# Performance work log

Hardware: AMD Instinct MI355X
Metric: run time of the kernel (lower is better)

The kernel has to match this reference:

```python
import jax, jax.numpy as jnp
import numpy as np

NEG_SLOPE = 0.2  # PyG GATConv default


def gat_conv(x, edge_index, W, a_src, a_dst, bias):
    """Single-head PyG-style GATConv (eval mode, add_self_loops=True)."""
    N = x.shape[0]
    h = x @ W  # [N, F_out]
    # add self loops
    loops = jnp.arange(N, dtype=edge_index.dtype)
    src = jnp.concatenate([edge_index[0], loops])  # [E+N]
    dst = jnp.concatenate([edge_index[1], loops])
    # per-edge attention logits: a_src . h_j + a_dst . h_i  (j=src, i=dst)
    alpha_s = h @ a_src  # [N]
    alpha_d = h @ a_dst  # [N]
    e = jax.nn.leaky_relu(alpha_s[src] + alpha_d[dst], NEG_SLOPE)  # [E+N]
    # segment softmax over incoming edges of each dst node
    m = jax.ops.segment_max(e, dst, num_segments=N)
    ex = jnp.exp(e - m[dst])
    denom = jax.ops.segment_sum(ex, dst, num_segments=N)
    alpha = ex / denom[dst]  # [E+N]
    # weighted scatter-aggregate of source features
    out = jax.ops.segment_sum(h[src] * alpha[:, None], dst, num_segments=N)
    return out + bias


def setup_inputs() -> dict:
    key = jax.random.key(0)
    ks = jax.random.split(key, 12)
    N, E = 100000, 3200000
    Fin, H, Fout = 128, 32, 32
    x = jax.random.normal(ks[0], (N, Fin), dtype=jnp.float32)
    edge_index = jax.random.randint(ks[1], (2, E), 0, N, dtype=jnp.int64)
    s = 1.0 / np.sqrt(Fin)
    W1 = jax.random.uniform(ks[2], (Fin, H), jnp.float32, -s, s)
    a1s = jax.random.uniform(ks[3], (H,), jnp.float32, -s, s)
    a1d = jax.random.uniform(ks[4], (H,), jnp.float32, -s, s)
    b1 = jnp.zeros((H,), jnp.float32)
    s2 = 1.0 / np.sqrt(H)
    W2 = jax.random.uniform(ks[5], (H, H), jnp.float32, -s2, s2)
    a2s = jax.random.uniform(ks[6], (H,), jnp.float32, -s2, s2)
    a2d = jax.random.uniform(ks[7], (H,), jnp.float32, -s2, s2)
    b2 = jnp.zeros((H,), jnp.float32)
    Wf = jax.random.uniform(ks[8], (H, Fout), jnp.float32, -s2, s2)
    bf = jax.random.uniform(ks[9], (Fout,), jnp.float32, -s2, s2)
    return {"x": x, "edge_index": edge_index, "W1": W1, "a1s": a1s, "a1d": a1d,
            "b1": b1, "W2": W2, "a2s": a2s, "a2d": a2d, "b2": b2,
            "Wf": Wf, "bf": bf}


def reference(x, edge_index, W1, a1s, a1d, b1, W2, a2s, a2d, b2, Wf, bf):
    h = jax.nn.relu(gat_conv(x, edge_index, W1, a1s, a1d, b1))
    h = jax.nn.relu(gat_conv(h, edge_index, W2, a2s, a2d, b2))
    return h @ Wf + bf
```

## Files before the change

kernel.cpp:

```cpp
#include <hip/hip_runtime.h>

#define NEG_SLOPE 0.2f
#define BK_LOG 9
#define BK_NODES (1 << BK_LOG)
#define TILE_EPT 24
#define TILE_E (256 * TILE_EPT)

typedef __attribute__((ext_vector_type(8))) short bf8_t;
typedef __attribute__((ext_vector_type(4))) float f32x4;

__device__ __forceinline__ float leaky(float v) { return v > 0.0f ? v : NEG_SLOPE * v; }

__device__ __forceinline__ unsigned short f2bf(float f) {
    unsigned u = __float_as_uint(f);
    u += 0x7fffu + ((u >> 16) & 1u);
    return (unsigned short)(u >> 16);
}
__device__ __forceinline__ float bf2f(unsigned short h) {
    return __uint_as_float(((unsigned)h) << 16);
}

__device__ __forceinline__ int scan256_excl(int v, int* tmp) {
    int t = threadIdx.x;
    tmp[t] = v;
    __syncthreads();
    for (int d = 1; d < 256; d <<= 1) {
        int x = (t >= d) ? tmp[t - d] : 0;
        __syncthreads();
        tmp[t] += x;
        __syncthreads();
    }
    int r = tmp[t] - v;
    __syncthreads();
    return r;
}

__device__ __forceinline__ void wsplit_body(int blk, int tid,
                                            const float* __restrict__ W,
                                            unsigned short* __restrict__ wh,
                                            unsigned short* __restrict__ wl, int K) {
    int idx = blk * 256 + tid;
    int KT = K >> 5;
    if (idx >= KT * 128) return;
    int lane = idx & 63;
    int nt = (idx >> 6) & 1;
    int kt = idx >> 7;
    int q = lane >> 4, c = lane & 15;
#pragma unroll
    for (int j = 0; j < 8; ++j) {
        int k = kt * 32 + q * 8 + j;
        int n = nt * 16 + c;
        float w = W[k * 32 + n];
        unsigned short hi = f2bf(w);
        wh[idx * 8 + j] = hi;
        wl[idx * 8 + j] = f2bf(w - bf2f(hi));
    }
}

__global__ __launch_bounds__(256) void k_prep(
    const float* __restrict__ W1, unsigned short* __restrict__ wh1, unsigned short* __restrict__ wl1,
    int* __restrict__ bcnt)
{
    int b = blockIdx.x, t = threadIdx.x;
    if (b < 2) wsplit_body(b, t, W1, wh1, wl1, 128);
    else       bcnt[t] = 0;
}

template <int FIN>
__device__ __forceinline__ void gemm_body(
    int blk, int tid,
    const float* __restrict__ x,
    const unsigned short* __restrict__ wh, const unsigned short* __restrict__ wl,
    const float* __restrict__ a_s, const float* __restrict__ a_d,
    float* __restrict__ h, float* __restrict__ alpha_s,
    float* __restrict__ alpha_d, int N)
{
    constexpr int KT = FIN / 32;
    int lane = tid & 63;
    int mt   = blk * 4 + (tid >> 6);
    int m0   = mt * 16;
    if (m0 >= N) return;
    int q = lane >> 4, c = lane & 15;

    bf8_t Bh[KT][2], Bl[KT][2];
#pragma unroll
    for (int kt = 0; kt < KT; ++kt)
#pragma unroll
        for (int nt = 0; nt < 2; ++nt) {
            Bh[kt][nt] = *(const bf8_t*)(wh + ((size_t)(kt * 2 + nt) * 64 + lane) * 8);
            Bl[kt][nt] = *(const bf8_t*)(wl + ((size_t)(kt * 2 + nt) * 64 + lane) * 8);
        }

    int rowa = m0 + c;
    if (rowa >= N) rowa = N - 1;
    const float* xr = x + (size_t)rowa * FIN;
    bf8_t Ah[KT], Al[KT];
#pragma unroll
    for (int kt = 0; kt < KT; ++kt) {
        f32x4 v0 = *(const f32x4*)(xr + kt * 32 + q * 8);
        f32x4 v1 = *(const f32x4*)(xr + kt * 32 + q * 8 + 4);
#pragma unroll
        for (int j = 0; j < 8; ++j) {
            float f = (j < 4) ? v0[j] : v1[j - 4];
            unsigned short hi = f2bf(f);
            Ah[kt][j] = (short)hi;
            Al[kt][j] = (short)f2bf(f - bf2f(hi));
        }
    }

    f32x4 acc0 = {0.f, 0.f, 0.f, 0.f}, acc1 = {0.f, 0.f, 0.f, 0.f};
#pragma unroll
    for (int kt = 0; kt < KT; ++kt) {
        acc0 = __builtin_amdgcn_mfma_f32_16x16x32_bf16(Ah[kt], Bh[kt][0], acc0, 0, 0, 0);
        acc1 = __builtin_amdgcn_mfma_f32_16x16x32_bf16(Ah[kt], Bh[kt][1], acc1, 0, 0, 0);
        acc0 = __builtin_amdgcn_mfma_f32_16x16x32_bf16(Al[kt], Bh[kt][0], acc0, 0, 0, 0);
        acc1 = __builtin_amdgcn_mfma_f32_16x16x32_bf16(Al[kt], Bh[kt][1], acc1, 0, 0, 0);
        acc0 = __builtin_amdgcn_mfma_f32_16x16x32_bf16(Ah[kt], Bl[kt][0], acc0, 0, 0, 0);
        acc1 = __builtin_amdgcn_mfma_f32_16x16x32_bf16(Ah[kt], Bl[kt][1], acc1, 0, 0, 0);
    }

#pragma unroll
    for (int reg = 0; reg < 4; ++reg) {
        int r = m0 + q * 4 + reg;
        if (r < N) {
            h[(size_t)r * 32 + c]      = acc0[reg];
            h[(size_t)r * 32 + 16 + c] = acc1[reg];
        }
    }
    float as0 = a_s[c], as1 = a_s[c + 16];
    float ad0 = a_d[c], ad1 = a_d[c + 16];
#pragma unroll
    for (int reg = 0; reg < 4; ++reg) {
        float ps = acc0[reg] * as0 + acc1[reg] * as1;
        float pd = acc0[reg] * ad0 + acc1[reg] * ad1;
#pragma unroll
        for (int msk = 8; msk >= 1; msk >>= 1) {
            ps += __shfl_xor(ps, msk);
            pd += __shfl_xor(pd, msk);
        }
        int r = m0 + q * 4 + reg;
        if (c == 0 && r < N) {
            alpha_s[r] = ps;
            alpha_d[r] = pd;
        }
    }
}

__global__ __launch_bounds__(256) void k_bcount_gemm1(
    const int* __restrict__ edst, int* __restrict__ bcnt, int E, int nb_tile,
    const float* __restrict__ x,
    const unsigned short* __restrict__ wh, const unsigned short* __restrict__ wl,
    const float* __restrict__ a_s, const float* __restrict__ a_d,
    float* __restrict__ h, float* __restrict__ alpha_s,
    float* __restrict__ alpha_d, int N)
{
    if ((int)blockIdx.x < nb_tile) {
        __shared__ int th[256];
        int t = threadIdx.x;
        th[t] = 0;
        __syncthreads();
        int base = blockIdx.x * TILE_E;
#pragma unroll
        for (int k = 0; k < TILE_EPT; ++k) {
            int e = base + t + k * 256;
            if (e < E) atomicAdd(&th[edst[e] >> BK_LOG], 1);
        }
        __syncthreads();
        if (th[t]) atomicAdd(&bcnt[t], th[t]);
    } else {
        gemm_body<128>(blockIdx.x - nb_tile, threadIdx.x, x, wh, wl,
                       a_s, a_d, h, alpha_s, alpha_d, N);
    }
}


__global__ __launch_bounds__(256) void k_bscan(const int* __restrict__ bcnt,
                                               int* __restrict__ bbase,
                                               int* __restrict__ bcur,
                                               int* __restrict__ off, int N, int E) {
    __shared__ int tmp[256];
    int t = threadIdx.x;
    int ex = scan256_excl(bcnt[t], tmp);
    bbase[t] = ex;
    bcur[t]  = ex;
    if (t == 0) { bbase[256] = E; off[N] = E; }
}

__global__ __launch_bounds__(256) void k_bplace(const int* __restrict__ esrc,
                                                const int* __restrict__ edst,
                                                int* __restrict__ bcur,
                                                unsigned* __restrict__ pairs, int E) {
    __shared__ int2 sp[TILE_E];
    __shared__ int th[256], tx[256], rb[256], tmp[256];
    int t = threadIdx.x;
    th[t] = 0;
    __syncthreads();
    int base = blockIdx.x * TILE_E;
    int tot  = min(TILE_E, E - base);
#pragma unroll
    for (int k = 0; k < TILE_EPT; ++k) {
        int e = base + t + k * 256;
        if (e < E) atomicAdd(&th[edst[e] >> BK_LOG], 1);
    }
    __syncthreads();
    int cnt = th[t];
    tx[t] = scan256_excl(cnt, tmp);
    rb[t] = atomicAdd(&bcur[t], cnt);
    th[t] = 0;
    __syncthreads();
#pragma unroll
    for (int k = 0; k < TILE_EPT; ++k) {
        int e = base + t + k * 256;
        if (e < E) {
            int s = esrc[e], d = edst[e];
            int b = d >> BK_LOG;
            int r = atomicAdd(&th[b], 1);
            sp[tx[b] + r] = make_int2(s, d);
        }
    }
    __syncthreads();
    for (int i = t; i < tot; i += 256) {
        int2 p = sp[i];
        int  b = p.y >> BK_LOG;
        pairs[rb[b] + (i - tx[b])] =
            ((unsigned)p.x << BK_LOG) | (unsigned)(p.y & (BK_NODES - 1));
    }
}

__global__ __launch_bounds__(512) void k_csr(const int* __restrict__ bbase,
                                             const unsigned* __restrict__ pairs,
                                             int* __restrict__ off,
                                             int* __restrict__ csr, int N) {
    __shared__ int lh[BK_NODES], lx[BK_NODES];
    int b = blockIdx.x, t = threadIdx.x;
    int lo = bbase[b], hi = bbase[b + 1];
    int node0 = b << BK_LOG;
    lh[t] = 0;
    __syncthreads();
    for (int j = lo + t; j < hi; j += 512)
        atomicAdd(&lh[pairs[j] & (BK_NODES - 1)], 1);
    __syncthreads();
    lx[t] = lh[t];
    __syncthreads();
    for (int d = 1; d < BK_NODES; d <<= 1) {
        int x0 = (t >= d) ? lx[t - d] : 0;
        __syncthreads();
        lx[t] += x0;
        __syncthreads();
    }
    lx[t] -= lh[t];
    if (node0 + t < N) off[node0 + t] = lo + lx[t];
    lh[t] = 0;
    __syncthreads();
    for (int j = lo + t; j < hi; j += 512) {
        unsigned p  = pairs[j];
        int      li = p & (BK_NODES - 1);
        int      r  = atomicAdd(&lh[li], 1);
        csr[lo + lx[li] + r] = (int)(p >> BK_LOG);
    }
}

template <bool FINAL>
__global__ __launch_bounds__(256) void fused_agg(
    const int* __restrict__ csr, const int* __restrict__ off,
    const float* __restrict__ alpha_s, const float* __restrict__ alpha_d,
    const float* __restrict__ h, const float* __restrict__ bias,
    const float* __restrict__ Wn,
    const float* __restrict__ an_s, const float* __restrict__ an_d,
    const float* __restrict__ bn,
    float* __restrict__ outh,
    float* __restrict__ out_as, float* __restrict__ out_ad, int N)
{
    int t = blockIdx.x * 256 + threadIdx.x;
    int i = t >> 3, q = t & 7;
    if (i >= N) return;
    int s0 = off[i], s1 = off[i + 1];
    float ad = alpha_d[i];

    const float* hq = h + q * 4;

    float w   = __expf(leaky(alpha_s[i] + ad));
    float den = w;
    f32x4 hv  = *(const f32x4*)(hq + (size_t)i * 32);
    f32x4 acc;
    acc[0] = w * hv[0]; acc[1] = w * hv[1]; acc[2] = w * hv[2]; acc[3] = w * hv[3];

    int   c0 = 0, c1 = 0, c2 = 0, c3 = 0;
    float a0 = 0.f, a1 = 0.f, a2 = 0.f, a3 = 0.f;
    {
        int i0 = s0 + q;
        c0 = (i0      < s1) ? csr[i0]      : 0;
        c1 = (i0 + 8  < s1) ? csr[i0 + 8]  : 0;
        c2 = (i0 + 16 < s1) ? csr[i0 + 16] : 0;
        c3 = (i0 + 24 < s1) ? csr[i0 + 24] : 0;
        a0 = alpha_s[c0]; a1 = alpha_s[c1]; a2 = alpha_s[c2]; a3 = alpha_s[c3];
    }
    for (int j = s0; j < s1; j += 32) {
        int jn = j + 32;
        int n0 = 0, n1 = 0, n2 = 0, n3 = 0;
        if (jn < s1) {
            int i0 = jn + q;
            n0 = (i0      < s1) ? csr[i0]      : 0;
            n1 = (i0 + 8  < s1) ? csr[i0 + 8]  : 0;
            n2 = (i0 + 16 < s1) ? csr[i0 + 16] : 0;
            n3 = (i0 + 24 < s1) ? csr[i0 + 24] : 0;
        }
        int i0 = j + q;
        float w0 = (i0      < s1) ? __expf(leaky(a0 + ad)) : 0.0f;
        float w1 = (i0 + 8  < s1) ? __expf(leaky(a1 + ad)) : 0.0f;
        float w2 = (i0 + 16 < s1) ? __expf(leaky(a2 + ad)) : 0.0f;
        float w3 = (i0 + 24 < s1) ? __expf(leaky(a3 + ad)) : 0.0f;
        float na0 = alpha_s[n0], na1 = alpha_s[n1];
        float na2 = alpha_s[n2], na3 = alpha_s[n3];
        int o0 = c0 << 5, o1 = c1 << 5, o2 = c2 << 5, o3 = c3 << 5;
#pragma unroll
        for (int e = 0; e < 8; ++e) {
            int   e0 = __shfl(o0, e, 8); float f0 = __shfl(w0, e, 8);
            int   e1 = __shfl(o1, e, 8); float f1 = __shfl(w1, e, 8);
            int   e2 = __shfl(o2, e, 8); float f2 = __shfl(w2, e, 8);
            int   e3 = __shfl(o3, e, 8); float f3 = __shfl(w3, e, 8);
            f32x4 g0 = *(const f32x4*)(hq + e0);
            f32x4 g1 = *(const f32x4*)(hq + e1);
            f32x4 g2 = *(const f32x4*)(hq + e2);
            f32x4 g3 = *(const f32x4*)(hq + e3);
            den += (f0 + f1) + (f2 + f3);
            acc[0] += f0 * g0[0]; acc[1] += f0 * g0[1];
            acc[2] += f0 * g0[2]; acc[3] += f0 * g0[3];
            acc[0] += f1 * g1[0]; acc[1] += f1 * g1[1];
            acc[2] += f1 * g1[2]; acc[3] += f1 * g1[3];
            acc[0] += f2 * g2[0]; acc[1] += f2 * g2[1];
            acc[2] += f2 * g2[2]; acc[3] += f2 * g2[3];
            acc[0] += f3 * g3[0]; acc[1] += f3 * g3[1];
            acc[2] += f3 * g3[2]; acc[3] += f3 * g3[3];
        }
        c0 = n0; c1 = n1; c2 = n2; c3 = n3;
        a0 = na0; a1 = na1; a2 = na2; a3 = na3;
    }

    float inv = 1.0f / den;
    f32x4 b4  = *(const f32x4*)(bias + q * 4);
    f32x4 r;
    r[0] = fmaxf(acc[0] * inv + b4[0], 0.0f);
    r[1] = fmaxf(acc[1] * inv + b4[1], 0.0f);
    r[2] = fmaxf(acc[2] * inv + b4[2], 0.0f);
    r[3] = fmaxf(acc[3] * inv + b4[3], 0.0f);

    f32x4 m = {0.f, 0.f, 0.f, 0.f};
#pragma unroll
    for (int e = 0; e < 8; ++e) {
        f32x4 rv;
        rv[0] = __shfl(r[0], e, 8);
        rv[1] = __shfl(r[1], e, 8);
        rv[2] = __shfl(r[2], e, 8);
        rv[3] = __shfl(r[3], e, 8);
#pragma unroll
        for (int jj = 0; jj < 4; ++jj) {
            f32x4 wr = *(const f32x4*)(Wn + (e * 4 + jj) * 32 + q * 4);
            m[0] += rv[jj] * wr[0]; m[1] += rv[jj] * wr[1];
            m[2] += rv[jj] * wr[2]; m[3] += rv[jj] * wr[3];
        }
    }

    if (FINAL) {
        f32x4 bb = *(const f32x4*)(bn + q * 4);
        m[0] += bb[0]; m[1] += bb[1]; m[2] += bb[2]; m[3] += bb[3];
        *(f32x4*)(outh + (size_t)i * 32 + q * 4) = m;
    } else {
        *(f32x4*)(outh + (size_t)i * 32 + q * 4) = m;
        f32x4 as4 = *(const f32x4*)(an_s + q * 4);
        f32x4 ad4 = *(const f32x4*)(an_d + q * 4);
        float ps = m[0] * as4[0] + m[1] * as4[1] + m[2] * as4[2] + m[3] * as4[3];
        float pd = m[0] * ad4[0] + m[1] * ad4[1] + m[2] * ad4[2] + m[3] * ad4[3];
#pragma unroll
        for (int msk = 4; msk >= 1; msk >>= 1) {
            ps += __shfl_xor(ps, msk, 8);
            pd += __shfl_xor(pd, msk, 8);
        }
        if (q == 0) { out_as[i] = ps; out_ad[i] = pd; }
    }
}

extern "C" void kernel_launch(void* const* d_in, const int* in_sizes, int n_in,
                              void* d_out, int out_size, void* d_ws, size_t ws_size,
                              hipStream_t stream)
{
    const float* x   = (const float*)d_in[0];
    const int*   ei  = (const int*)d_in[1];
    const float* W1  = (const float*)d_in[2];
    const float* a1s = (const float*)d_in[3];
    const float* a1d = (const float*)d_in[4];
    const float* b1  = (const float*)d_in[5];
    const float* W2  = (const float*)d_in[6];
    const float* a2s = (const float*)d_in[7];
    const float* a2d = (const float*)d_in[8];
    const float* b2  = (const float*)d_in[9];
    const float* Wf  = (const float*)d_in[10];
    const float* bf  = (const float*)d_in[11];

    const int N = in_sizes[0] / 128;
    const int E = in_sizes[1] / 2;
    const int* esrc = ei;
    const int* edst = ei + E;
    const int B1 = (N + BK_NODES - 1) >> BK_LOG;

    float* ws = (float*)d_ws;
    float* h1       = ws;
    float* h2       = h1 + (size_t)N * 32;
    float* alpha_s  = h2 + (size_t)N * 32;
    float* alpha_d  = alpha_s + N;
    float* alpha_s2 = alpha_d + N;
    float* alpha_d2 = alpha_s2 + N;
    int*   off      = (int*)(alpha_d2 + N);
    int*   csr      = off + (N + 1);
    int*   bcnt     = csr + E;
    int*   bbase    = bcnt + 256;
    int*   bcur     = bbase + 257;
    unsigned short* wfb =
        (unsigned short*)(((uintptr_t)(bcur + 256) + 15) & ~(uintptr_t)15);
    unsigned short* wh1 = wfb;
    unsigned short* wl1 = wh1 + 4096;
    unsigned* pairs = ((size_t)E <= (size_t)32 * N)
                          ? (unsigned*)h2
                          : (unsigned*)(wl1 + 4096);

    const int nb_agg  = (N * 8 + 255) / 256;
    const int nb_tile = (E + TILE_E - 1) / TILE_E;
    const int nb_gemm = ((N + 15) / 16 + 3) / 4;

    k_prep<<<3, 256, 0, stream>>>(W1, wh1, wl1, bcnt);

    k_bcount_gemm1<<<nb_tile + nb_gemm, 256, 0, stream>>>(
        edst, bcnt, E, nb_tile, x, wh1, wl1, a1s, a1d, h1, alpha_s, alpha_d, N);

    k_bscan  <<<1, 256, 0, stream>>>(bcnt, bbase, bcur, off, N, E);
    k_bplace <<<nb_tile, 256, 0, stream>>>(esrc, edst, bcur, pairs, E);
    k_csr    <<<B1, 512, 0, stream>>>(bbase, pairs, off, csr, N);

    fused_agg<false><<<nb_agg, 256, 0, stream>>>(
        csr, off, alpha_s, alpha_d, h1, b1, W2, a2s, a2d, nullptr,
        h2, alpha_s2, alpha_d2, N);

    fused_agg<true><<<nb_agg, 256, 0, stream>>>(
        csr, off, alpha_s2, alpha_d2, h2, b2, Wf, nullptr, nullptr, bf,
        (float*)d_out, nullptr, nullptr, N);
}
```

Baseline: 338.4 us.

## Vectorize edge bucketing loads, drop LDS staging in placement, simplify aggregation prefetch

The bucket-count and placement kernels now read edge indices as int4 vectors. The placement kernel no longer stages pairs in a large shared buffer and writes them straight to global memory at atomically assigned slots. Dropping the staging cuts LDS use, which may raise occupancy, but gives up coalesced output writes. The aggregation kernel also removes its software prefetch of the next CSR and alpha chunk, trading latency hiding for fewer registers.

```diff
diff --git a/kernel.cpp b/kernel.cpp
--- a/kernel.cpp
+++ b/kernel.cpp
@@ -160,10 +160,22 @@
         th[t] = 0;
         __syncthreads();
         int base = blockIdx.x * TILE_E;
-#pragma unroll
-        for (int k = 0; k < TILE_EPT; ++k) {
-            int e = base + t + k * 256;
-            if (e < E) atomicAdd(&th[edst[e] >> BK_LOG], 1);
+        int rem  = min(TILE_E, E - base);
+        if ((E & 3) == 0) {
+            const int4* ed4 = (const int4*)(edst + base);
+            int nv = rem >> 2;
+            for (int k = t; k < nv; k += 256) {
+                int4 d = ed4[k];
+                atomicAdd(&th[d.x >> BK_LOG], 1);
+                atomicAdd(&th[d.y >> BK_LOG], 1);
+                atomicAdd(&th[d.z >> BK_LOG], 1);
+                atomicAdd(&th[d.w >> BK_LOG], 1);
+            }
+            for (int e = (nv << 2) + t; e < rem; e += 256)
+                atomicAdd(&th[edst[base + e] >> BK_LOG], 1);
+        } else {
+            for (int e = t; e < rem; e += 256)
+                atomicAdd(&th[edst[base + e] >> BK_LOG], 1);
         }
         __syncthreads();
         if (th[t]) atomicAdd(&bcnt[t], th[t]);
@@ -190,40 +202,61 @@
                                                 const int* __restrict__ edst,
                                                 int* __restrict__ bcur,
                                                 unsigned* __restrict__ pairs, int E) {
-    __shared__ int2 sp[TILE_E];
-    __shared__ int th[256], tx[256], rb[256], tmp[256];
+    __shared__ int th[256], rb[256];
     int t = threadIdx.x;
     th[t] = 0;
     __syncthreads();
     int base = blockIdx.x * TILE_E;
-    int tot  = min(TILE_E, E - base);
-#pragma unroll
-    for (int k = 0; k < TILE_EPT; ++k) {
-        int e = base + t + k * 256;
-        if (e < E) atomicAdd(&th[edst[e] >> BK_LOG], 1);
+    int rem  = min(TILE_E, E - base);
+    bool vec = ((E & 3) == 0);
+    if (vec) {
+        const int4* ed4 = (const int4*)(edst + base);
+        int nv = rem >> 2;
+        for (int k = t; k < nv; k += 256) {
+            int4 d = ed4[k];
+            atomicAdd(&th[d.x >> BK_LOG], 1);
+            atomicAdd(&th[d.y >> BK_LOG], 1);
+            atomicAdd(&th[d.z >> BK_LOG], 1);
+            atomicAdd(&th[d.w >> BK_LOG], 1);
+        }
+        for (int e = (nv << 2) + t; e < rem; e += 256)
+            atomicAdd(&th[edst[base + e] >> BK_LOG], 1);
+    } else {
+        for (int e = t; e < rem; e += 256)
+            atomicAdd(&th[edst[base + e] >> BK_LOG], 1);
     }
     __syncthreads();
     int cnt = th[t];
-    tx[t] = scan256_excl(cnt, tmp);
-    rb[t] = atomicAdd(&bcur[t], cnt);
+    if (cnt) rb[t] = atomicAdd(&bcur[t], cnt);
     th[t] = 0;
     __syncthreads();
-#pragma unroll
-    for (int k = 0; k < TILE_EPT; ++k) {
-        int e = base + t + k * 256;
-        if (e < E) {
-            int s = esrc[e], d = edst[e];
-            int b = d >> BK_LOG;
-            int r = atomicAdd(&th[b], 1);
-            sp[tx[b] + r] = make_int2(s, d);
-        }
-    }
-    __syncthreads();
-    for (int i = t; i < tot; i += 256) {
-        int2 p = sp[i];
-        int  b = p.y >> BK_LOG;
-        pairs[rb[b] + (i - tx[b])] =
-            ((unsigned)p.x << BK_LOG) | (unsigned)(p.y & (BK_NODES - 1));
+    if (vec) {
+        const int4* ed4 = (const int4*)(edst + base);
+        const int4* es4 = (const int4*)(esrc + base);
+        int nv = rem >> 2;
+        for (int k = t; k < nv; k += 256) {
+            int4 d = ed4[k];
+            int4 s = es4[k];
+            int b0 = d.x >> BK_LOG, r0 = atomicAdd(&th[b0], 1);
+            pairs[rb[b0] + r0] = ((unsigned)s.x << BK_LOG) | (unsigned)(d.x & (BK_NODES - 1));
+            int b1 = d.y >> BK_LOG, r1 = atomicAdd(&th[b1], 1);
+            pairs[rb[b1] + r1] = ((unsigned)s.y << BK_LOG) | (unsigned)(d.y & (BK_NODES - 1));
+            int b2 = d.z >> BK_LOG, r2 = atomicAdd(&th[b2], 1);
+            pairs[rb[b2] + r2] = ((unsigned)s.z << BK_LOG) | (unsigned)(d.z & (BK_NODES - 1));
+            int b3 = d.w >> BK_LOG, r3 = atomicAdd(&th[b3], 1);
+            pairs[rb[b3] + r3] = ((unsigned)s.w << BK_LOG) | (unsigned)(d.w & (BK_NODES - 1));
+        }
+        for (int e = (nv << 2) + t; e < rem; e += 256) {
+            int d = edst[base + e], s = esrc[base + e];
+            int b = d >> BK_LOG, r = atomicAdd(&th[b], 1);
+            pairs[rb[b] + r] = ((unsigned)s << BK_LOG) | (unsigned)(d & (BK_NODES - 1));
+        }
+    } else {
+        for (int e = t; e < rem; e += 256) {
+            int d = edst[base + e], s = esrc[base + e];
+            int b = d >> BK_LOG, r = atomicAdd(&th[b], 1);
+            pairs[rb[b] + r] = ((unsigned)s << BK_LOG) | (unsigned)(d & (BK_NODES - 1));
+        }
     }
 }
 
@@ -285,33 +318,20 @@
     f32x4 acc;
     acc[0] = w * hv[0]; acc[1] = w * hv[1]; acc[2] = w * hv[2]; acc[3] = w * hv[3];
 
-    int   c0 = 0, c1 = 0, c2 = 0, c3 = 0;
-    float a0 = 0.f, a1 = 0.f, a2 = 0.f, a3 = 0.f;
-    {
-        int i0 = s0 + q;
-        c0 = (i0      < s1) ? csr[i0]      : 0;
-        c1 = (i0 + 8  < s1) ? csr[i0 + 8]  : 0;
-        c2 = (i0 + 16 < s1) ? csr[i0 + 16] : 0;
-        c3 = (i0 + 24 < s1) ? csr[i0 + 24] : 0;
-        a0 = alpha_s[c0]; a1 = alpha_s[c1]; a2 = alpha_s[c2]; a3 = alpha_s[c3];
-    }
     for (int j = s0; j < s1; j += 32) {
-        int jn = j + 32;
-        int n0 = 0, n1 = 0, n2 = 0, n3 = 0;
-        if (jn < s1) {
-            int i0 = jn + q;
-            n0 = (i0      < s1) ? csr[i0]      : 0;
-            n1 = (i0 + 8  < s1) ? csr[i0 + 8]  : 0;
-            n2 = (i0 + 16 < s1) ? csr[i0 + 16] : 0;
-            n3 = (i0 + 24 < s1) ? csr[i0 + 24] : 0;
-        }
-        int i0 = j + q;
-        float w0 = (i0      < s1) ? __expf(leaky(a0 + ad)) : 0.0f;
-        float w1 = (i0 + 8  < s1) ? __expf(leaky(a1 + ad)) : 0.0f;
-        float w2 = (i0 + 16 < s1) ? __expf(leaky(a2 + ad)) : 0.0f;
-        float w3 = (i0 + 24 < s1) ? __expf(leaky(a3 + ad)) : 0.0f;
-        float na0 = alpha_s[n0], na1 = alpha_s[n1];
-        float na2 = alpha_s[n2], na3 = alpha_s[n3];
+        int i0 = j + q, i1 = i0 + 8, i2 = i0 + 16, i3 = i0 + 24;
+        int c0 = (i0 < s1) ? csr[i0] : 0;
+        int c1 = (i1 < s1) ? csr[i1] : 0;
+        int c2 = (i2 < s1) ? csr[i2] : 0;
+        int c3 = (i3 < s1) ? csr[i3] : 0;
+        float e0x = __expf(leaky(alpha_s[c0] + ad));
+        float e1x = __expf(leaky(alpha_s[c1] + ad));
+        float e2x = __expf(leaky(alpha_s[c2] + ad));
+        float e3x = __expf(leaky(alpha_s[c3] + ad));
+        float w0 = (i0 < s1) ? e0x : 0.0f;
+        float w1 = (i1 < s1) ? e1x : 0.0f;
+        float w2 = (i2 < s1) ? e2x : 0.0f;
+        float w3 = (i3 < s1) ? e3x : 0.0f;
         int o0 = c0 << 5, o1 = c1 << 5, o2 = c2 << 5, o3 = c3 << 5;
 #pragma unroll
         for (int e = 0; e < 8; ++e) {
@@ -333,8 +353,6 @@
             acc[0] += f3 * g3[0]; acc[1] += f3 * g3[1];
             acc[2] += f3 * g3[2]; acc[3] += f3 * g3[3];
         }
-        c0 = n0; c1 = n1; c2 = n2; c3 = n3;
-        a0 = na0; a1 = na1; a2 = na2; a3 = na3;
     }
 
     float inv = 1.0f / den;
```

After: 342.9 us. About the same (+1.3%).
